# Kernel optimization log

Hardware: AMD Instinct MI355X
Metric: run time of the kernel (lower is better)

## Reference

```python
import jax, jax.numpy as jnp
import numpy as np

THRESHOLD = 0.35      # overlap_thresh
NEGPOS_RATIO = 7
VAR0, VAR1 = 0.1, 0.2  # self.variance


def make_priors():
    # Standard RetinaFace 640x640 anchor grid -> 16800 priors (cx, cy, w, h)
    img = 640
    steps = [8, 16, 32]
    min_sizes = [[16, 32], [64, 128], [256, 512]]
    out = []
    for step, ms in zip(steps, min_sizes):
        f = img // step
        ii, jj = np.meshgrid(np.arange(f), np.arange(f), indexing="ij")
        cx = ((jj + 0.5) * step / img).ravel().astype(np.float32)
        cy = ((ii + 0.5) * step / img).ravel().astype(np.float32)
        for m in ms:
            s = np.full_like(cx, m / img)
            out.append(np.stack([cx, cy, s, s], axis=-1))
    return jnp.asarray(np.concatenate(out, axis=0), dtype=jnp.float32)


def jaccard(a, b):
    # a: [O,4] point-form gt boxes, b: [P,4] point-form priors -> IoU [O,P]
    lt = jnp.maximum(a[:, None, :2], b[None, :, :2])
    rb = jnp.minimum(a[:, None, 2:], b[None, :, 2:])
    wh = jnp.clip(rb - lt, 0.0)
    inter = wh[..., 0] * wh[..., 1]
    area_a = ((a[:, 2] - a[:, 0]) * (a[:, 3] - a[:, 1]))[:, None]
    area_b = ((b[:, 2] - b[:, 0]) * (b[:, 3] - b[:, 1]))[None, :]
    return inter / (area_a + area_b - inter)


def setup_inputs() -> dict:
    key = jax.random.key(0)
    ks = jax.random.split(key, 7)
    B, P, O = 64, 16800, 64
    loc_data = jax.random.normal(ks[0], (B, P, 4), jnp.float32)
    conf_data = jax.random.normal(ks[1], (B, P, 2), jnp.float32)
    landm_data = jax.random.normal(ks[2], (B, P, 10), jnp.float32)
    priors = make_priors()
    # targets: [B, O, 15] = [xmin ymin xmax ymax | 10 landmark coords | label]
    c = jax.random.uniform(ks[3], (B, O, 2), minval=0.15, maxval=0.85)
    wh = jax.random.uniform(ks[4], (B, O, 2), minval=0.05, maxval=0.3)
    boxes = jnp.concatenate([jnp.clip(c - wh / 2, 1e-3, 0.999),
                             jnp.clip(c + wh / 2, 1e-3, 0.999)], axis=-1)
    landms = jax.random.uniform(ks[5], (B, O, 10))
    lab = jnp.where(jax.random.uniform(ks[6], (B, O, 1)) < 0.8, 1.0, -1.0)
    targets = jnp.concatenate([boxes, landms, lab], axis=-1).astype(jnp.float32)
    return {"loc_data": loc_data, "conf_data": conf_data,
            "landm_data": landm_data, "priors": priors, "targets": targets}


def _smooth_l1(x):
    ax = jnp.abs(x)
    return jnp.where(ax < 1.0, 0.5 * ax * ax, ax - 0.5)


def reference(loc_data, conf_data, landm_data, priors, targets):
    B, P, C = conf_data.shape
    O = targets.shape[1]
    priors_pf = jnp.concatenate([priors[:, :2] - priors[:, 2:] * 0.5,
                                 priors[:, :2] + priors[:, 2:] * 0.5], axis=1)

    def match_one(t):
        truths = t[:, :4]
        landms = t[:, 4:14]
        labels = t[:, 14].astype(jnp.int32)
        ov = jaccard(truths, priors_pf)               # [O,P]
        bp_ov = ov.max(axis=1)                         # best prior per truth
        bp_idx = jnp.argmax(ov, axis=1)
        valid = bp_ov >= 0.2                           # RetinaFace gt filter
        bt_ov = ov.max(axis=0)                         # best truth per prior
        bt_idx = jnp.argmax(ov, axis=0)
        # index_fill_(best_prior_idx, 2) for valid gts, ensure best prior kept
        bt_ov = bt_ov.at[bp_idx].set(jnp.where(valid, 2.0, bt_ov[bp_idx]))
        bt_idx = bt_idx.at[bp_idx].set(jnp.arange(O))
        matched = truths[bt_idx]                       # [P,4] point form
        conf = labels[bt_idx]
        conf = jnp.where(bt_ov < THRESHOLD, 0, conf)
        # encode loc target
        g_cxcy = ((matched[:, :2] + matched[:, 2:]) * 0.5 - priors[:, :2]) / (VAR0 * priors[:, 2:])
        g_wh = jnp.log((matched[:, 2:] - matched[:, :2]) / priors[:, 2:]) / VAR1
        loc = jnp.concatenate([g_cxcy, g_wh], axis=1)
        # encode landmark target (5 points)
        ml = landms[bt_idx].reshape(P, 5, 2)
        lm = ((ml - priors[:, None, :2]) / (VAR0 * priors[:, None, 2:])).reshape(P, 10)
        any_valid = jnp.any(valid)                     # early-return branch of match()
        return (jnp.where(any_valid, loc, 0.0),
                jnp.where(any_valid, conf, 0),
                jnp.where(any_valid, lm, 0.0))

    loc_t, conf_t, landm_t = jax.vmap(match_one)(targets)
    loc_t = jax.lax.stop_gradient(loc_t)       # targets built from .data in torch
    landm_t = jax.lax.stop_gradient(landm_t)

    # landmark loss over conf_t > 0
    pos1 = conf_t > 0
    N1 = jnp.maximum(pos1.sum().astype(jnp.float32), 1.0)
    loss_landm = jnp.sum(jnp.where(pos1[..., None], _smooth_l1(landm_data - landm_t), 0.0))

    # localization loss over conf_t != 0 (labels -1 and 1 both positive)
    pos = conf_t != 0
    conf_t1 = jnp.where(pos, 1, conf_t)        # conf_t[pos] = 1 -> values in {0,1}
    loss_l = jnp.sum(jnp.where(pos[..., None], _smooth_l1(loc_data - loc_t), 0.0))

    # hard negative mining
    lse = jax.nn.logsumexp(conf_data, axis=2)                       # [B,P]
    picked = jnp.take_along_axis(conf_data, conf_t1[..., None], axis=2)[..., 0]
    ce_all = lse - picked                                            # per-anchor CE
    rank_score = jnp.where(pos, 0.0, ce_all)
    loss_idx = jnp.argsort(-rank_score, axis=1)
    idx_rank = jnp.argsort(loss_idx, axis=1)
    num_pos = pos.sum(axis=1, keepdims=True)
    num_neg = jnp.minimum(NEGPOS_RATIO * num_pos, P - 1)
    neg = idx_rank < num_neg
    union = pos | neg
    loss_c = jnp.sum(jnp.where(union, ce_all, 0.0))

    N = jnp.maximum(num_pos.sum().astype(jnp.float32), 1.0)
    return loss_l / N, loss_c / N, loss_landm / N1
```

## Files before the change

kernel.cpp:

```cpp
#include <hip/hip_runtime.h>
#include <math.h>

#define B 64
#define P 16800
#define O 64
#define THRESH 0.35f
#define VALID_T 0.2f
#define HB 2048
#define HSHIFT 21
#define AREA_M 0.34f
#define CCAP 4096
#define MULT 2
#define RPB 2
#define CHB (MULT * 256)
#define NB2 ((P + CHB - 1) / CHB)
#define KD1B ((B / RPB) * NB2)
#define KCEB (B * 4)
#define KB2B (B * O / 4)
#define QG (P / 4 / 4)

__device__ __forceinline__ float smooth_l1(float x) {
    float ax = fabsf(x);
    return ax < 1.f ? 0.5f * ax * ax : ax - 0.5f;
}
__device__ __forceinline__ float lse2(float c0, float c1) {
    float m = fmaxf(c0, c1);
    return m + __logf(__expf(c0 - m) + __expf(c1 - m));
}
__device__ __forceinline__ void iou_upd(float4 t, float area_a,
                                        float px1, float py1, float px2, float py2,
                                        float area_b,
                                        float& bnum, float& bden, int& bio, int o) {
    float w = fmaxf(fminf(t.z, px2) - fmaxf(t.x, px1), 0.f);
    float h = fmaxf(fminf(t.w, py2) - fmaxf(t.y, py1), 0.f);
    float inter = w * h;
    float den = area_a + area_b - inter;
    if (inter * bden > bnum * den) { bnum = inter; bden = den; bio = o; }
}
__device__ __forceinline__ float wave_sum(float v) {
#pragma unroll
    for (int s = 32; s > 0; s >>= 1) v += __shfl_down(v, s, 64);
    return v;
}
__device__ __forceinline__ int wave_sum_i(int v) {
#pragma unroll
    for (int s = 32; s > 0; s >>= 1) v += __shfl_down(v, s, 64);
    return v;
}
__device__ __forceinline__ float wave_min(float v) {
#pragma unroll
    for (int s = 32; s > 0; s >>= 1) v = fminf(v, __shfl_xor(v, s, 64));
    return v;
}
__device__ __forceinline__ float wave_max(float v) {
#pragma unroll
    for (int s = 32; s > 0; s >>= 1) v = fmaxf(v, __shfl_xor(v, s, 64));
    return v;
}
__device__ __forceinline__ int wave_sufscan(int v, int lane) {
#pragma unroll
    for (int s = 1; s < 64; s <<= 1) {
        int o = __shfl_down(v, s, 64);
        if (lane + s < 64) v += o;
    }
    return v;
}
__device__ __forceinline__ void wave0_select(const int* h, int nb, int k,
                                             int* s_bin, int* s_kk, int tid) {
    if (tid >= 64) return;
    int lane = tid;
    int bpl = (nb + 63) >> 6;
    int b0 = lane * bpl;
    int s = 0;
    for (int i = 0; i < bpl; ++i) { int bb = b0 + i; if (bb < nb) s += h[bb]; }
    int suf = wave_sufscan(s, lane);
    int sufn = __shfl_down(suf, 1, 64);
    if (lane == 63) sufn = 0;
    if (suf >= k && sufn < k) {
        int cum = sufn;
        for (int i = bpl - 1; i >= 0; --i) {
            int bb = b0 + i; if (bb >= nb) continue;
            int hv = h[bb];
            if (cum + hv >= k) { *s_bin = bb; *s_kk = k - cum; break; }
            cum += hv;
        }
    }
}

__global__ void __launch_bounds__(256) kMain(
        const float* __restrict__ loc_data, const float* __restrict__ conf_data,
        const float* __restrict__ landm_data, const float* __restrict__ priors,
        const float* __restrict__ targets,
        unsigned char* __restrict__ pflag, float* __restrict__ rank,
        int* __restrict__ hist,
        int* __restrict__ num_pos,
        float* __restrict__ gsum, int* __restrict__ np1_tot,
        unsigned long long* __restrict__ bp_final) {
    if (blockIdx.x >= KD1B + KCEB) {
        int pair = (blockIdx.x - KD1B - KCEB) * 4 + (threadIdx.x >> 6);
        int lane = threadIdx.x & 63;
        int o = pair & (O - 1);
        int b = pair >> 6;
        const float* tt = &targets[(b * O + o) * 15];
        float tx1 = tt[0], ty1 = tt[1], tx2 = tt[2], ty2 = tt[3];
        float area_a = (tx2 - tx1) * (ty2 - ty1);
        float4 tb = make_float4(tx1, ty1, tx2, ty2);
        float bn = 0.f, bd = 1.f;
        unsigned bp = 0u;
        const int fs[6]   = {80, 80, 40, 40, 20, 20};
        const int ms[6]   = {16, 32, 64, 128, 256, 512};
        const int base[6] = {0, 6400, 12800, 14400, 16000, 16400};
#pragma unroll
        for (int c = 0; c < 6; ++c) {
            int f = fs[c];
            float inv = (float)f;
            float h = (float)ms[c] * (0.5f / 640.f);
            int j0 = (int)floorf((tx1 - h) * inv - 0.5f) - 1; if (j0 < 0) j0 = 0;
            int j1 = (int)ceilf((tx2 + h) * inv - 0.5f) + 1;  if (j1 > f - 1) j1 = f - 1;
            int i0 = (int)floorf((ty1 - h) * inv - 0.5f) - 1; if (i0 < 0) i0 = 0;
            int i1 = (int)ceilf((ty2 + h) * inv - 0.5f) + 1;  if (i1 > f - 1) i1 = f - 1;
            if (j1 < j0 || i1 < i0) continue;
            int nj = j1 - j0 + 1;
            int n = (i1 - i0 + 1) * nj;
            float rcp_nj = 1.0f / (float)nj;
            for (int idx = lane; idx < n; idx += 64) {
                int ii = (int)((float)idx * rcp_nj);
                int jj = idx - ii * nj;
                if (jj < 0) { ii--; jj += nj; } else if (jj >= nj) { ii++; jj -= nj; }
                int p = base[c] + (i0 + ii) * f + (j0 + jj);
                float4 q = ((const float4*)priors)[p];
                float px1 = q.x - q.z * 0.5f, py1 = q.y - q.w * 0.5f;
                float px2 = q.x + q.z * 0.5f, py2 = q.y + q.w * 0.5f;
                float areab = (px2 - px1) * (py2 - py1);
                float w = fmaxf(fminf(tb.z, px2) - fmaxf(tb.x, px1), 0.f);
                float hh = fmaxf(fminf(tb.w, py2) - fmaxf(tb.y, py1), 0.f);
                float inter = w * hh;
                float den = area_a + areab - inter;
                float l = bn * den, r = inter * bd;
                if (r > l) { bn = inter; bd = den; bp = (unsigned)p; }
            }
        }
#pragma unroll
        for (int s = 32; s > 0; s >>= 1) {
            float no = __shfl_xor(bn, s, 64), dd = __shfl_xor(bd, s, 64);
            unsigned po = __shfl_xor(bp, s, 64);
            float l = bn * dd, r = no * bd;
            bool take = (r > l) || (r == l && po < bp);
            if (take) { bn = no; bd = dd; bp = po; }
        }
        if (lane == 0) {
            float iou = bn / bd;
            bp_final[b * O + o] = ((unsigned long long)__float_as_uint(iou) << 32)
                                | (unsigned)(0xFFFFFFFFu - bp);
        }
        return;
    }
    if (blockIdx.x >= KD1B) {
        int cb = blockIdx.x - KD1B;
        int b = cb >> 2, q = cb & 3;
        __shared__ int lhist[HB];
        int tid = threadIdx.x;
        for (int i = tid; i < HB; i += 256) lhist[i] = 0;
        __syncthreads();
        const float4* c4 = (const float4*)(conf_data + (size_t)b * P * 2);
        uint4* r4 = (uint4*)(rank + (size_t)b * P);
        for (int i = tid; i < QG; i += 256) {
            int e = q * QG + i;
            float4 a = c4[2 * e];
            float4 c = c4[2 * e + 1];
            unsigned u0 = __float_as_uint(lse2(a.x, a.y) - a.x);
            unsigned u1 = __float_as_uint(lse2(a.z, a.w) - a.z);
            unsigned u2 = __float_as_uint(lse2(c.x, c.y) - c.x);
            unsigned u3 = __float_as_uint(lse2(c.z, c.w) - c.z);
            r4[e] = make_uint4(u0, u1, u2, u3);
            atomicAdd(&lhist[u0 >> HSHIFT], 1);
            atomicAdd(&lhist[u1 >> HSHIFT], 1);
            atomicAdd(&lhist[u2 >> HSHIFT], 1);
            atomicAdd(&lhist[u3 >> HSHIFT], 1);
        }
        __syncthreads();
        int* gh = hist + (size_t)b * HB;
        for (int i = tid; i < HB; i += 256) {
            int cgt = lhist[i];
            if (cgt) atomicAdd(&gh[i], cgt);
        }
        return;
    }
    int blk = blockIdx.x % NB2;
    int rp = blockIdx.x / NB2;
    int p0 = blk * CHB;
    __shared__ float traw[O * 15];
    __shared__ float4 t4[O];
    __shared__ float ta[O], lab[O];
    __shared__ float wredf[2][4];
    __shared__ int wredi[2][4];
    int tid = threadIdx.x;
    int wid = tid >> 6, lid = tid & 63;
    float px1[MULT], py1[MULT], px2[MULT], py2[MULT], areab[MULT];
    float4 pr4[MULT];
    bool act[MULT];
    float cbx1[MULT], cby1[MULT], cbx2[MULT], cby2[MULT], camn[MULT], camx[MULT];
#pragma unroll
    for (int mi = 0; mi < MULT; ++mi) {
        int p = p0 + mi * 256 + tid;
        act[mi] = (p < P);
        int pc = act[mi] ? p : (P - 1);
        float4 q = ((const float4*)priors)[pc];
        pr4[mi] = q;
        px1[mi] = q.x - q.z * 0.5f; py1[mi] = q.y - q.w * 0.5f;
        px2[mi] = q.x + q.z * 0.5f; py2[mi] = q.y + q.w * 0.5f;
        areab[mi] = (px2[mi] - px1[mi]) * (py2[mi] - py1[mi]);
        cbx1[mi] = wave_min(px1[mi]); cby1[mi] = wave_min(py1[mi]);
        cbx2[mi] = wave_max(px2[mi]); cby2[mi] = wave_max(py2[mi]);
        camn[mi] = wave_min(areab[mi]); camx[mi] = wave_max(areab[mi]);
    }
    for (int r = 0; r < RPB; ++r) {
        int b = rp * RPB + r;
        __syncthreads();
        if (tid < O * 15 / 4)
            ((float4*)traw)[tid] = ((const float4*)(targets + (size_t)b * O * 15))[tid];
        __syncthreads();
        if (tid < 64) {
            const float* tr = &traw[tid * 15];
            float a0 = tr[0], a1 = tr[1], a2 = tr[2], a3 = tr[3];
            t4[tid] = make_float4(a0, a1, a2, a3);
            ta[tid] = (a2 - a0) * (a3 - a1);
            lab[tid] = tr[14];
        }
        __syncthreads();
        float4 tl = t4[lid];
        float Aal = ta[lid];
        unsigned long long mk[MULT];
#pragma unroll
        for (int mi = 0; mi < MULT; ++mi) {
            bool pass = (fminf(tl.z, cbx2[mi]) - fmaxf(tl.x, cbx1[mi]) > 0.f) &&
                        (fminf(tl.w, cby2[mi]) - fmaxf(tl.y, cby1[mi]) > 0.f) &&
                        (Aal >= AREA_M * camn[mi]) && (camx[mi] >= AREA_M * Aal);
            mk[mi] = __ballot(pass);
        }
        float bnum[MULT], bden[MULT]; int bi[MULT];
#pragma unroll
        for (int mi = 0; mi < MULT; ++mi) {
            bnum[mi] = 0.f; bden[mi] = 1.f; bi[mi] = 0;
            unsigned long long mm = mk[mi];
            float Ap = areab[mi];
            while (mm) {
                int o = __ffsll(mm) - 1;
                mm &= mm - 1;
                float4 t = t4[o];
                float Aa = ta[o];
                if (Aa >= AREA_M * Ap && Ap >= AREA_M * Aa)
                    iou_upd(t, Aa, px1[mi], py1[mi], px2[mi], py2[mi], Ap,
                            bnum[mi], bden[mi], bi[mi], o);
            }
        }
        float ll = 0.f, llm = 0.f;
        int cp = 0, cp1 = 0;
#pragma unroll
        for (int mi = 0; mi < MULT; ++mi) {
            if (!act[mi]) continue;
            int p = p0 + mi * 256 + tid;
            float best = bnum[mi] / bden[mi];
            int conf = (best >= THRESH) ? (int)lab[bi[mi]] : 0;
            bool pos = conf != 0;
            pflag[(size_t)b * P + p] = pos ? 1 : 0;
            if (pos) {
                cp++;
                int ti = bi[mi];
                float cx = pr4[mi].x, cy = pr4[mi].y, sw = pr4[mi].z, sh = pr4[mi].w;
                float4 t = t4[ti];
                float gx = ((t.x + t.z) * 0.5f - cx) / (0.1f * sw);
                float gy = ((t.y + t.w) * 0.5f - cy) / (0.1f * sh);
                float gw = logf((t.z - t.x) / sw) / 0.2f;
                float gh = logf((t.w - t.y) / sh) / 0.2f;
                const float* ld = &loc_data[(size_t)(b * P + p) * 4];
                ll += smooth_l1(ld[0] - gx) + smooth_l1(ld[1] - gy) +
                      smooth_l1(ld[2] - gw) + smooth_l1(ld[3] - gh);
                if (conf > 0) {
                    cp1++;
                    const float* lmd = &landm_data[(size_t)(b * P + p) * 10];
                    const float* lmt = &traw[ti * 15 + 4];
                    for (int k5 = 0; k5 < 5; ++k5) {
                        float lx = (lmt[k5 * 2 + 0] - cx) / (0.1f * sw);
                        float ly = (lmt[k5 * 2 + 1] - cy) / (0.1f * sh);
                        llm += smooth_l1(lmd[k5 * 2 + 0] - lx) + smooth_l1(lmd[k5 * 2 + 1] - ly);
                    }
                }
            }
        }
        float s_ll = wave_sum(ll), s_llm = wave_sum(llm);
        int s_cp = wave_sum_i(cp), s_cp1 = wave_sum_i(cp1);
        if (lid == 0) {
            wredf[0][wid] = s_ll; wredf[1][wid] = s_llm;
            wredi[0][wid] = s_cp; wredi[1][wid] = s_cp1;
        }
        __syncthreads();
        if (tid == 0) {
            float ll_t = wredf[0][0] + wredf[0][1] + wredf[0][2] + wredf[0][3];
            float llm_t = wredf[1][0] + wredf[1][1] + wredf[1][2] + wredf[1][3];
            int cp_t = wredi[0][0] + wredi[0][1] + wredi[0][2] + wredi[0][3];
            int cp1_t = wredi[1][0] + wredi[1][1] + wredi[1][2] + wredi[1][3];
            if (ll_t != 0.f)  atomicAdd(&gsum[0], ll_t);
            if (llm_t != 0.f) atomicAdd(&gsum[1], llm_t);
            if (cp_t)  atomicAdd(&num_pos[b], cp_t);
            if (cp1_t) atomicAdd(np1_tot, cp1_t);
        }
    }
}

__global__ void __launch_bounds__(1024) kTail(
        const float* __restrict__ priors, const float* __restrict__ targets,
        const float* __restrict__ loc_data, const float* __restrict__ conf_data,
        const float* __restrict__ landm_data,
        const unsigned long long* __restrict__ bp_final,
        const unsigned char* __restrict__ pflag,
        const float* __restrict__ rank, const int* __restrict__ hist,
        const int* __restrict__ num_pos,
        float* __restrict__ gsum, int* __restrict__ np1_tot, int* __restrict__ np_tot,
        float* __restrict__ lossc_tot, int* __restrict__ done,
        float* __restrict__ out) {
    __shared__ __align__(16) unsigned lrow[P];
    __shared__ int lh[HB];
    __shared__ float4 t4[O];
    __shared__ float ta[O], lab[O];
    __shared__ int sp[O];
    __shared__ int hist2[256];
    __shared__ unsigned lcand[CCAP];
    __shared__ int s_np, s_bin0, s_kk0, s_bin, s_kk, s_cnt;
    __shared__ float wredf[16];
    __shared__ int wredi[16];
    __shared__ float s_cepw[16];
    __shared__ float s_sumgt;

    int b = blockIdx.x;
    int tid = threadIdx.x;
    int lane = tid & 63;
    int wv = tid >> 6;
    for (int i = tid; i < HB; i += 1024) lh[i] = hist[(size_t)b * HB + i];
    if (tid == 0) s_cnt = 0;
    int p = 0, v = 0;
    if (tid < O) {
        const float* tt = &targets[(b * O + tid) * 15];
        float4 tj = make_float4(tt[0], tt[1], tt[2], tt[3]);
        t4[tid] = tj;
        ta[tid] = (tj.z - tj.x) * (tj.w - tj.y);
        lab[tid] = tt[14];
        unsigned long long kpk = bp_final[b * O + tid];
        p = (int)(0xFFFFFFFFu - (unsigned)(kpk & 0xFFFFFFFFu));
        float iou = __uint_as_float((unsigned)(kpk >> 32));
        v = (iou >= VALID_T) ? 1 : 0;
        sp[tid] = p;
    }
    const uint4* r4 = (const uint4*)(rank + (size_t)b * P);
    for (int i = tid; i < P / 4; i += 1024) ((uint4*)lrow)[i] = r4[i];
    __syncthreads();
    const uchar4* f4v = (const uchar4*)(pflag + (size_t)b * P);
    const float2* cf2 = (const float2*)(conf_data + (size_t)b * P * 2);
    float cep = 0.f;
    for (int i = tid; i < P / 4; i += 1024) {
        uchar4 fl = f4v[i];
        if (fl.x | fl.y | fl.z | fl.w) {
#pragma unroll
            for (int kq = 0; kq < 4; ++kq) {
                unsigned char f = (kq == 0) ? fl.x : (kq == 1) ? fl.y : (kq == 2) ? fl.z : fl.w;
                if (f) {
                    int pp = i * 4 + kq;
                    unsigned old = lrow[pp];
                    lrow[pp] = 0u;
                    atomicAdd(&lh[old >> HSHIFT], -1);
                    atomicAdd(&lh[0], 1);
                    float2 cc = cf2[pp];
                    cep += lse2(cc.x, cc.y) - cc.y;
                }
            }
        }
    }
    {
        float sc = wave_sum(cep);
        if (lane == 0) s_cepw[wv] = sc;
    }
    __syncthreads();
    int dnp = 0, dn1 = 0;
    float dll = 0.f, dllm = 0.f, dce = 0.f;
    if (tid < O) {
        int j = tid;
        bool winner = true;
        for (int jj = j + 1; jj < O; ++jj)
            if (sp[jj] == p) { winner = false; break; }
        if (winner) {
            float4 q = ((const float4*)priors)[p];
            float px1 = q.x - q.z * 0.5f, py1 = q.y - q.w * 0.5f;
            float px2 = q.x + q.z * 0.5f, py2 = q.y + q.w * 0.5f;
            float areab = (px2 - px1) * (py2 - py1);
            float bnum = 0.f, bden = 1.f; int bi = 0;
            for (int o = 0; o < O; ++o) {
                float Aa = ta[o];
                if (Aa >= AREA_M * areab && areab >= AREA_M * Aa)
                    iou_upd(t4[o], Aa, px1, py1, px2, py2, areab, bnum, bden, bi, o);
            }
            float best = bnum / bden;
            float ov_new = v ? 2.0f : best;
            int conf_old = (best >= THRESH) ? (int)lab[bi] : 0;
            int conf_new = (ov_new >= THRESH) ? (int)lab[j] : 0;
            float2 c01 = ((const float2*)conf_data)[b * P + p];
            float c0 = c01.x, c1 = c01.y;
            float lse = lse2(c0, c1);
            bool po = conf_old != 0, pn = conf_new != 0;
            float ceo = lse - (po ? c1 : c0), cen = lse - (pn ? c1 : c0);
            float rvo = po ? 0.f : ceo, rvn = pn ? 0.f : cen;
            if (__float_as_uint(rvo) != __float_as_uint(rvn)) {
                lrow[p] = __float_as_uint(rvn);
                int bo = __float_as_uint(rvo) >> HSHIFT, bn = __float_as_uint(rvn) >> HSHIFT;
                if (bo != bn) { atomicAdd(&lh[bn], 1); atomicAdd(&lh[bo], -1); }
            }
            const float* ld = &loc_data[(size_t)(b * P + p) * 4];
            auto enc_ll = [&](int ti) -> float {
                float4 t = t4[ti];
                float gx = ((t.x + t.z) * 0.5f - q.x) / (0.1f * q.z);
                float gy = ((t.y + t.w) * 0.5f - q.y) / (0.1f * q.w);
                float gw = logf((t.z - t.x) / q.z) / 0.2f;
                float gh = logf((t.w - t.y) / q.w) / 0.2f;
                return smooth_l1(ld[0] - gx) + smooth_l1(ld[1] - gy) +
                       smooth_l1(ld[2] - gw) + smooth_l1(ld[3] - gh);
            };
            if (po) dll -= enc_ll(bi);
            if (pn) dll += enc_ll(j);
            dce = (pn ? cen : 0.f) - (po ? ceo : 0.f);
            dnp = (int)pn - (int)po;
            const float* lmd = &landm_data[(size_t)(b * P + p) * 10];
            auto enc_lm = [&](int ti) -> float {
                const float* lmt = &targets[(b * O + ti) * 15 + 4];
                float sum = 0.f;
                for (int k5 = 0; k5 < 5; ++k5) {
                    float lx = (lmt[k5 * 2 + 0] - q.x) / (0.1f * q.z);
                    float ly = (lmt[k5 * 2 + 1] - q.y) / (0.1f * q.w);
                    sum += smooth_l1(lmd[k5 * 2 + 0] - lx) + smooth_l1(lmd[k5 * 2 + 1] - ly);
                }
                return sum;
            };
            if (conf_old > 0) dllm -= enc_lm(bi);
            if (conf_new > 0) dllm += enc_lm(j);
            dn1 = (int)(conf_new > 0) - (int)(conf_old > 0);
        }
    }
    float pce_reg = 0.f;
    if (tid < 64) {
        float r_ll = wave_sum(dll), r_lm = wave_sum(dllm), r_ce = wave_sum(dce);
        int r_np = wave_sum_i(dnp), r_n1 = wave_sum_i(dn1);
        if (tid == 0) {
            if (r_ll != 0.f) atomicAdd(&gsum[0], r_ll);
            if (r_lm != 0.f) atomicAdd(&gsum[1], r_lm);
            float cep_tot = 0.f;
            for (int i = 0; i < 16; ++i) cep_tot += s_cepw[i];
            pce_reg = cep_tot + r_ce;
            int np = num_pos[b] + r_np;
            s_np = np;
            atomicAdd(np_tot, np);
            if (r_n1) atomicAdd(np1_tot, r_n1);
        }
    }
    __syncthreads();
    int k = s_np * 7;
    if (k > P - 1) k = P - 1;
    if (tid == 0) { s_bin0 = (k <= 0) ? -1 : 0; s_kk0 = (k <= 0) ? 0 : k; }
    if (k > 0) wave0_select(lh, HB, k, &s_bin0, &s_kk0, tid);
    __syncthreads();
    int bin = s_bin0;
    int kk0 = s_kk0;
    float topk_b = 0.f;
    if (bin >= 0) {
        if (tid < 256) hist2[tid] = 0;
        __syncthreads();
        unsigned lo_bound = ((unsigned)(bin + 1)) << HSHIFT;
        float sumgt = 0.f;
        for (int i = tid; i < P / 4; i += 1024) {
            uint4 u4 = ((const uint4*)lrow)[i];
#define TAIL_H(u) { if ((u) >= lo_bound) sumgt += __uint_as_float(u); \
                    else if (((u) >> HSHIFT) == (unsigned)bin) { \
                        int idx = atomicAdd(&s_cnt, 1); \
                        if (idx < CCAP) lcand[idx] = (u); \
                        atomicAdd(&hist2[((u) >> 13) & 255], 1); } }
            TAIL_H(u4.x) TAIL_H(u4.y) TAIL_H(u4.z) TAIL_H(u4.w)
#undef TAIL_H
        }
        float sg = wave_sum(sumgt);
        if (lane == 0) wredf[wv] = sg;
        __syncthreads();
        if (tid == 0) {
            float t = 0.f;
            for (int i = 0; i < 16; ++i) t += wredf[i];
            s_sumgt = t;
        }
        wave0_select(hist2, 256, kk0, &s_bin, &s_kk, tid);
        __syncthreads();
        unsigned pref = (((unsigned)bin) << HSHIFT) | (((unsigned)s_bin) << 13);
        unsigned resolved = (0xFFFFFFFFu << HSHIFT) | (255u << 13);
        int kk = s_kk;
        int m = s_cnt;
        bool useG = (m > CCAP);
        for (int pass = 0; pass < 2; ++pass) {
            int sh = pass == 0 ? 5 : 0;
            int nb = pass == 0 ? 256 : 32;
            if (tid < nb) hist2[tid] = 0;
            __syncthreads();
            if (!useG) {
                for (int i = tid; i < m; i += 1024) {
                    unsigned u = lcand[i];
                    if ((u & resolved) == pref) atomicAdd(&hist2[(u >> sh) & (nb - 1)], 1);
                }
            } else {
                for (int pp = tid; pp < P; pp += 1024) {
                    unsigned u = lrow[pp];
                    if ((u & resolved) == pref) atomicAdd(&hist2[(u >> sh) & (nb - 1)], 1);
                }
            }
            __syncthreads();
            wave0_select(hist2, nb, kk, &s_bin, &s_kk, tid);
            __syncthreads();
            pref |= ((unsigned)s_bin) << sh;
            resolved |= (unsigned)(nb - 1) << sh;
            kk = s_kk;
        }
        float tv = __uint_as_float(pref);
        float sumS = 0.f; int cntS = 0;
        for (int pp = tid; pp < P; pp += 1024) {
            unsigned u = lrow[pp];
            if ((u >> HSHIFT) == (unsigned)bin) {
                float val = __uint_as_float(u);
                if (val > tv) { sumS += val; cntS++; }
            }
        }
        float s2 = wave_sum(sumS); int c2 = wave_sum_i(cntS);
        if (lane == 0) { wredf[wv] = s2; wredi[wv] = c2; }
        __syncthreads();
        if (tid == 0) {
            float st = 0.f; int ct = 0;
            for (int i = 0; i < 16; ++i) { st += wredf[i]; ct += wredi[i]; }
            topk_b = s_sumgt + st + (float)(kk0 - ct) * tv;
        }
    }
    if (tid == 0) {
        atomicAdd(lossc_tot, pce_reg + topk_b);
        __threadfence();
        int old = atomicAdd(done, 1);
        if (old == B - 1) {
            float g0 = atomicAdd(&gsum[0], 0.f);
            float g1 = atomicAdd(&gsum[1], 0.f);
            float lc = atomicAdd(lossc_tot, 0.f);
            int np = atomicAdd(np_tot, 0);
            int n1 = atomicAdd(np1_tot, 0);
            float N = fmaxf((float)np, 1.f);
            float N1 = fmaxf((float)n1, 1.f);
            out[0] = g0 / N;
            out[1] = lc / N;
            out[2] = g1 / N1;
        }
    }
}

extern "C" void kernel_launch(void* const* d_in, const int* in_sizes, int n_in,
                              void* d_out, int out_size, void* d_ws, size_t ws_size,
                              hipStream_t stream) {
    const float* loc_data   = (const float*)d_in[0];
    const float* conf_data  = (const float*)d_in[1];
    const float* landm_data = (const float*)d_in[2];
    const float* priors     = (const float*)d_in[3];
    const float* targets    = (const float*)d_in[4];
    float* out = (float*)d_out;

    char* ws = (char*)d_ws;
    size_t off = 0;
    auto alloc = [&](size_t bytes) -> void* {
        void* pp = ws + off;
        off += (bytes + 255) & ~(size_t)255;
        return pp;
    };
    float* rank     = (float*)alloc((size_t)B * P * 4);
    unsigned char* pflag = (unsigned char*)alloc((size_t)B * P);
    unsigned long long* bp_final = (unsigned long long*)alloc((size_t)B * O * 8);
    size_t hist_bytes = (size_t)B * HB * 4;
    char* zbase = (char*)alloc(hist_bytes);
    int* hist = (int*)zbase;
    size_t acc_bytes = (size_t)(B * 4 + 64);
    char* acc = (char*)alloc(acc_bytes);
    int*   num_pos      = (int*)acc;
    float* gsum         = (float*)(acc + B * 4);
    int*   np1_tot      = (int*)(acc + B * 4 + 8);
    int*   np_tot       = (int*)(acc + B * 4 + 12);
    float* lossc_tot    = (float*)(acc + B * 4 + 16);
    int*   done         = (int*)(acc + B * 4 + 20);
    size_t zlen = (size_t)((acc + acc_bytes) - zbase);

    hipMemsetAsync(zbase, 0, zlen, stream);
    kMain<<<dim3(KD1B + KCEB + KB2B), dim3(256), 0, stream>>>(
        loc_data, conf_data, landm_data, priors, targets,
        pflag, rank, hist, num_pos, gsum, np1_tot, bp_final);
    kTail<<<dim3(B), dim3(1024), 0, stream>>>(priors, targets, loc_data, conf_data,
                                              landm_data, bp_final, pflag, rank, hist,
                                              num_pos, gsum, np1_tot, np_tot,
                                              lossc_tot, done, out);
}
```

Before: 168.1 us.

## Split per-batch tail kernel into fix, segmented scan, and resolve kernels

The single 64-block, 1024-thread tail kernel used to stage a whole rank row in shared memory. It is replaced by three kernels: a 256-thread fix-up kernel that patches rank/pflag in global memory and picks the coarse bin, a scan kernel that spreads the threshold-bin scan over 16 segments per batch row (1024 blocks) with ballot-aggregated candidate compaction into global memory, and a resolve kernel that finishes the radix select from the compacted candidates. This exposes far more parallelism for the full-row scan and lowers per-block shared memory, at the cost of two extra launches and extra global traffic and atomics.

```diff
diff --git a/kernel.cpp b/kernel.cpp
--- a/kernel.cpp
+++ b/kernel.cpp
@@ -18,6 +18,8 @@
 #define KCEB (B * 4)
 #define KB2B (B * O / 4)
 #define QG (P / 4 / 4)
+#define SSEG 16
+#define SLEN (P / SSEG)
 
 __device__ __forceinline__ float smooth_l1(float x) {
     float ax = fabsf(x);
@@ -308,36 +310,26 @@
     }
 }
 
-__global__ void __launch_bounds__(1024) kTail(
+__global__ void __launch_bounds__(256) kFixBin(
         const float* __restrict__ priors, const float* __restrict__ targets,
         const float* __restrict__ loc_data, const float* __restrict__ conf_data,
         const float* __restrict__ landm_data,
         const unsigned long long* __restrict__ bp_final,
-        const unsigned char* __restrict__ pflag,
-        const float* __restrict__ rank, const int* __restrict__ hist,
+        unsigned char* __restrict__ pflag, float* __restrict__ rank,
+        const int* __restrict__ hist,
         const int* __restrict__ num_pos,
         float* __restrict__ gsum, int* __restrict__ np1_tot, int* __restrict__ np_tot,
-        float* __restrict__ lossc_tot, int* __restrict__ done,
-        float* __restrict__ out) {
-    __shared__ __align__(16) unsigned lrow[P];
+        float* __restrict__ pos_ce, int* __restrict__ binArr, int* __restrict__ kkArr) {
     __shared__ int lh[HB];
     __shared__ float4 t4[O];
     __shared__ float ta[O], lab[O];
     __shared__ int sp[O];
-    __shared__ int hist2[256];
-    __shared__ unsigned lcand[CCAP];
-    __shared__ int s_np, s_bin0, s_kk0, s_bin, s_kk, s_cnt;
-    __shared__ float wredf[16];
-    __shared__ int wredi[16];
-    __shared__ float s_cepw[16];
-    __shared__ float s_sumgt;
-
+    __shared__ float s_cepw[4];
+    __shared__ int s_np, s_bin0, s_kk0;
     int b = blockIdx.x;
     int tid = threadIdx.x;
-    int lane = tid & 63;
-    int wv = tid >> 6;
-    for (int i = tid; i < HB; i += 1024) lh[i] = hist[(size_t)b * HB + i];
-    if (tid == 0) s_cnt = 0;
+    int lane = tid & 63, wv = tid >> 6;
+    for (int i = tid; i < HB; i += 256) lh[i] = hist[(size_t)b * HB + i];
     int p = 0, v = 0;
     if (tid < O) {
         const float* tt = &targets[(b * O + tid) * 15];
@@ -351,13 +343,12 @@
         v = (iou >= VALID_T) ? 1 : 0;
         sp[tid] = p;
     }
-    const uint4* r4 = (const uint4*)(rank + (size_t)b * P);
-    for (int i = tid; i < P / 4; i += 1024) ((uint4*)lrow)[i] = r4[i];
     __syncthreads();
     const uchar4* f4v = (const uchar4*)(pflag + (size_t)b * P);
+    const float* rrow = rank + (size_t)b * P;
     const float2* cf2 = (const float2*)(conf_data + (size_t)b * P * 2);
     float cep = 0.f;
-    for (int i = tid; i < P / 4; i += 1024) {
+    for (int i = tid; i < P / 4; i += 256) {
         uchar4 fl = f4v[i];
         if (fl.x | fl.y | fl.z | fl.w) {
 #pragma unroll
@@ -365,8 +356,7 @@
                 unsigned char f = (kq == 0) ? fl.x : (kq == 1) ? fl.y : (kq == 2) ? fl.z : fl.w;
                 if (f) {
                     int pp = i * 4 + kq;
-                    unsigned old = lrow[pp];
-                    lrow[pp] = 0u;
+                    unsigned old = __float_as_uint(rrow[pp]);
                     atomicAdd(&lh[old >> HSHIFT], -1);
                     atomicAdd(&lh[0], 1);
                     float2 cc = cf2[pp];
@@ -409,7 +399,8 @@
             float ceo = lse - (po ? c1 : c0), cen = lse - (pn ? c1 : c0);
             float rvo = po ? 0.f : ceo, rvn = pn ? 0.f : cen;
             if (__float_as_uint(rvo) != __float_as_uint(rvn)) {
-                lrow[p] = __float_as_uint(rvn);
+                rank[(size_t)b * P + p] = cen;
+                pflag[(size_t)b * P + p] = pn ? 1 : 0;
                 int bo = __float_as_uint(rvo) >> HSHIFT, bn = __float_as_uint(rvn) >> HSHIFT;
                 if (bo != bn) { atomicAdd(&lh[bn], 1); atomicAdd(&lh[bo], -1); }
             }
@@ -443,16 +434,14 @@
             dn1 = (int)(conf_new > 0) - (int)(conf_old > 0);
         }
     }
-    float pce_reg = 0.f;
     if (tid < 64) {
         float r_ll = wave_sum(dll), r_lm = wave_sum(dllm), r_ce = wave_sum(dce);
         int r_np = wave_sum_i(dnp), r_n1 = wave_sum_i(dn1);
         if (tid == 0) {
             if (r_ll != 0.f) atomicAdd(&gsum[0], r_ll);
             if (r_lm != 0.f) atomicAdd(&gsum[1], r_lm);
-            float cep_tot = 0.f;
-            for (int i = 0; i < 16; ++i) cep_tot += s_cepw[i];
-            pce_reg = cep_tot + r_ce;
+            float cep_tot = s_cepw[0] + s_cepw[1] + s_cepw[2] + s_cepw[3];
+            pos_ce[b] = cep_tot + r_ce;
             int np = num_pos[b] + r_np;
             s_np = np;
             atomicAdd(np_tot, np);
@@ -463,59 +452,113 @@
     int k = s_np * 7;
     if (k > P - 1) k = P - 1;
     if (tid == 0) { s_bin0 = (k <= 0) ? -1 : 0; s_kk0 = (k <= 0) ? 0 : k; }
+    __syncthreads();
     if (k > 0) wave0_select(lh, HB, k, &s_bin0, &s_kk0, tid);
     __syncthreads();
-    int bin = s_bin0;
-    int kk0 = s_kk0;
+    if (tid == 0) { binArr[b] = s_bin0; kkArr[b] = s_kk0; }
+}
+
+__global__ void __launch_bounds__(256) kScan(
+        const float* __restrict__ rank, const unsigned char* __restrict__ pflag,
+        const int* __restrict__ binArr,
+        float* __restrict__ sumgt_part, unsigned* __restrict__ cand,
+        int* __restrict__ cand_cnt, int* __restrict__ h1) {
+    int seg = blockIdx.x % SSEG;
+    int b = blockIdx.x / SSEG;
+    int bin = binArr[b];
+    if (bin < 0) return;
+    __shared__ float wred[4];
+    int t = threadIdx.x;
+    int lane = t & 63, wv = t >> 6;
+    unsigned lo_bound = ((unsigned)(bin + 1)) << HSHIFT;
+    const float* r = rank + (size_t)b * P;
+    const unsigned char* f = pflag + (size_t)b * P;
+    int* hrow = h1 + b * 256;
+    float sumgt = 0.f;
+    int pend = (seg + 1) * SLEN;
+    for (int p = seg * SLEN + t; p < pend; p += 256) {
+        unsigned u = f[p] ? 0u : __float_as_uint(r[p]);
+        bool gt = u >= lo_bound;
+        bool inb = !gt && ((u >> HSHIFT) == (unsigned)bin);
+        if (gt) sumgt += __uint_as_float(u);
+        unsigned long long mkb = __ballot(inb);
+        if (mkb) {
+            unsigned long long act = __ballot(true);
+            int ldr = __ffsll(act) - 1;
+            int cnt = __popcll(mkb);
+            int bas = 0;
+            if (lane == ldr) bas = atomicAdd(&cand_cnt[b], cnt);
+            bas = __shfl(bas, ldr, 64);
+            if (inb) {
+                int pos = bas + __popcll(mkb & ((1ull << lane) - 1ull));
+                if (pos < CCAP) cand[(size_t)b * CCAP + pos] = u;
+                atomicAdd(&hrow[(u >> 13) & 255], 1);
+            }
+        }
+    }
+    float sg = wave_sum(sumgt);
+    if (lane == 0) wred[wv] = sg;
+    __syncthreads();
+    if (t == 0) {
+        float tot = wred[0] + wred[1] + wred[2] + wred[3];
+        if (tot != 0.f) atomicAdd(&sumgt_part[b], tot);
+    }
+}
+
+__global__ void __launch_bounds__(256) kResolve(
+        const float* __restrict__ rank, const unsigned char* __restrict__ pflag,
+        const unsigned* __restrict__ cand, const int* __restrict__ cand_cnt,
+        const int* __restrict__ binArr, const int* __restrict__ kkArr,
+        const float* __restrict__ sumgt_part, const int* __restrict__ h1,
+        const float* __restrict__ pos_ce,
+        float* __restrict__ gsum, int* __restrict__ np_tot, int* __restrict__ np1_tot,
+        float* __restrict__ lossc_tot, int* __restrict__ done,
+        float* __restrict__ out) {
+    __shared__ unsigned lcand[CCAP];
+    __shared__ int hist2[256];
+    __shared__ int s_bin, s_kk;
+    __shared__ float wredf[4];
+    __shared__ int wredi[4];
+    int b = blockIdx.x;
+    int t = threadIdx.x;
+    int lane = t & 63, wv = t >> 6;
+    int bin = binArr[b];
     float topk_b = 0.f;
     if (bin >= 0) {
-        if (tid < 256) hist2[tid] = 0;
-        __syncthreads();
-        unsigned lo_bound = ((unsigned)(bin + 1)) << HSHIFT;
-        float sumgt = 0.f;
-        for (int i = tid; i < P / 4; i += 1024) {
-            uint4 u4 = ((const uint4*)lrow)[i];
-#define TAIL_H(u) { if ((u) >= lo_bound) sumgt += __uint_as_float(u); \
-                    else if (((u) >> HSHIFT) == (unsigned)bin) { \
-                        int idx = atomicAdd(&s_cnt, 1); \
-                        if (idx < CCAP) lcand[idx] = (u); \
-                        atomicAdd(&hist2[((u) >> 13) & 255], 1); } }
-            TAIL_H(u4.x) TAIL_H(u4.y) TAIL_H(u4.z) TAIL_H(u4.w)
-#undef TAIL_H
-        }
-        float sg = wave_sum(sumgt);
-        if (lane == 0) wredf[wv] = sg;
-        __syncthreads();
-        if (tid == 0) {
-            float t = 0.f;
-            for (int i = 0; i < 16; ++i) t += wredf[i];
-            s_sumgt = t;
-        }
-        wave0_select(hist2, 256, kk0, &s_bin, &s_kk, tid);
+        int m = cand_cnt[b];
+        int kk0 = kkArr[b];
+        bool useG = (m > CCAP);
+        const float* r = rank + (size_t)b * P;
+        const unsigned char* f = pflag + (size_t)b * P;
+        if (!useG) {
+            int mm = m;
+            for (int i = t; i < mm; i += 256) lcand[i] = cand[(size_t)b * CCAP + i];
+        }
+        if (t < 256) hist2[t] = h1[b * 256 + t];
+        __syncthreads();
+        wave0_select(hist2, 256, kk0, &s_bin, &s_kk, t);
         __syncthreads();
         unsigned pref = (((unsigned)bin) << HSHIFT) | (((unsigned)s_bin) << 13);
         unsigned resolved = (0xFFFFFFFFu << HSHIFT) | (255u << 13);
         int kk = s_kk;
-        int m = s_cnt;
-        bool useG = (m > CCAP);
         for (int pass = 0; pass < 2; ++pass) {
             int sh = pass == 0 ? 5 : 0;
             int nb = pass == 0 ? 256 : 32;
-            if (tid < nb) hist2[tid] = 0;
+            if (t < nb) hist2[t] = 0;
             __syncthreads();
             if (!useG) {
-                for (int i = tid; i < m; i += 1024) {
+                for (int i = t; i < m; i += 256) {
                     unsigned u = lcand[i];
                     if ((u & resolved) == pref) atomicAdd(&hist2[(u >> sh) & (nb - 1)], 1);
                 }
             } else {
-                for (int pp = tid; pp < P; pp += 1024) {
-                    unsigned u = lrow[pp];
+                for (int pp = t; pp < P; pp += 256) {
+                    unsigned u = f[pp] ? 0u : __float_as_uint(r[pp]);
                     if ((u & resolved) == pref) atomicAdd(&hist2[(u >> sh) & (nb - 1)], 1);
                 }
             }
             __syncthreads();
-            wave0_select(hist2, nb, kk, &s_bin, &s_kk, tid);
+            wave0_select(hist2, nb, kk, &s_bin, &s_kk, t);
             __syncthreads();
             pref |= ((unsigned)s_bin) << sh;
             resolved |= (unsigned)(nb - 1) << sh;
@@ -523,24 +566,31 @@
         }
         float tv = __uint_as_float(pref);
         float sumS = 0.f; int cntS = 0;
-        for (int pp = tid; pp < P; pp += 1024) {
-            unsigned u = lrow[pp];
-            if ((u >> HSHIFT) == (unsigned)bin) {
-                float val = __uint_as_float(u);
+        if (!useG) {
+            for (int i = t; i < m; i += 256) {
+                float val = __uint_as_float(lcand[i]);
                 if (val > tv) { sumS += val; cntS++; }
+            }
+        } else {
+            for (int pp = t; pp < P; pp += 256) {
+                unsigned u = f[pp] ? 0u : __float_as_uint(r[pp]);
+                if ((u >> HSHIFT) == (unsigned)bin) {
+                    float val = __uint_as_float(u);
+                    if (val > tv) { sumS += val; cntS++; }
+                }
             }
         }
         float s2 = wave_sum(sumS); int c2 = wave_sum_i(cntS);
         if (lane == 0) { wredf[wv] = s2; wredi[wv] = c2; }
         __syncthreads();
-        if (tid == 0) {
-            float st = 0.f; int ct = 0;
-            for (int i = 0; i < 16; ++i) { st += wredf[i]; ct += wredi[i]; }
-            topk_b = s_sumgt + st + (float)(kk0 - ct) * tv;
-        }
-    }
-    if (tid == 0) {
-        atomicAdd(lossc_tot, pce_reg + topk_b);
+        if (t == 0) {
+            float st = wredf[0] + wredf[1] + wredf[2] + wredf[3];
+            int ct = wredi[0] + wredi[1] + wredi[2] + wredi[3];
+            topk_b = sumgt_part[b] + st + (float)(kk0 - ct) * tv;
+        }
+    }
+    if (t == 0) {
+        atomicAdd(lossc_tot, pos_ce[b] + topk_b);
         __threadfence();
         int old = atomicAdd(done, 1);
         if (old == B - 1) {
@@ -578,25 +628,40 @@
     float* rank     = (float*)alloc((size_t)B * P * 4);
     unsigned char* pflag = (unsigned char*)alloc((size_t)B * P);
     unsigned long long* bp_final = (unsigned long long*)alloc((size_t)B * O * 8);
+    unsigned* cand  = (unsigned*)alloc((size_t)B * CCAP * 4);
+    int* binArr     = (int*)alloc(B * 4);
+    int* kkArr      = (int*)alloc(B * 4);
     size_t hist_bytes = (size_t)B * HB * 4;
     char* zbase = (char*)alloc(hist_bytes);
     int* hist = (int*)zbase;
-    size_t acc_bytes = (size_t)(B * 4 + 64);
-    char* acc = (char*)alloc(acc_bytes);
+    size_t rest_bytes = (size_t)(B * 256 * 4 + 3 * B * 4 + B * 4 + 64);
+    char* zr = (char*)alloc(rest_bytes);
+    int*   h1         = (int*)zr;
+    float* sumgt_part = (float*)(zr + B * 256 * 4);
+    int*   cand_cnt   = (int*)(zr + B * 256 * 4 + B * 4);
+    float* pos_ce     = (float*)(zr + B * 256 * 4 + 2 * B * 4);
+    char*  acc        = zr + B * 256 * 4 + 3 * B * 4;
     int*   num_pos      = (int*)acc;
-    float* gsum         = (float*)(acc + B * 4);
-    int*   np1_tot      = (int*)(acc + B * 4 + 8);
-    int*   np_tot       = (int*)(acc + B * 4 + 12);
-    float* lossc_tot    = (float*)(acc + B * 4 + 16);
-    int*   done         = (int*)(acc + B * 4 + 20);
-    size_t zlen = (size_t)((acc + acc_bytes) - zbase);
+    float* gsum         = (float*)(acc);
+    int*   np1_tot      = (int*)(acc + 8);
+    int*   np_tot       = (int*)(acc + 12);
+    float* lossc_tot    = (float*)(acc + 16);
+    int*   done         = (int*)(acc + 20);
+    (void)num_pos;
+    char* zb2 = (char*)alloc((size_t)B * 4);
+    int* num_pos2 = (int*)zb2;
+    size_t zlen = (size_t)((zb2 + B * 4) - zbase);
 
     hipMemsetAsync(zbase, 0, zlen, stream);
     kMain<<<dim3(KD1B + KCEB + KB2B), dim3(256), 0, stream>>>(
         loc_data, conf_data, landm_data, priors, targets,
-        pflag, rank, hist, num_pos, gsum, np1_tot, bp_final);
-    kTail<<<dim3(B), dim3(1024), 0, stream>>>(priors, targets, loc_data, conf_data,
-                                              landm_data, bp_final, pflag, rank, hist,
-                                              num_pos, gsum, np1_tot, np_tot,
-                                              lossc_tot, done, out);
-}
+        pflag, rank, hist, num_pos2, gsum, np1_tot, bp_final);
+    kFixBin<<<dim3(B), dim3(256), 0, stream>>>(
+        priors, targets, loc_data, conf_data, landm_data, bp_final,
+        pflag, rank, hist, num_pos2, gsum, np1_tot, np_tot, pos_ce, binArr, kkArr);
+    kScan<<<dim3(B * SSEG), dim3(256), 0, stream>>>(
+        rank, pflag, binArr, sumgt_part, cand, cand_cnt, h1);
+    kResolve<<<dim3(B), dim3(256), 0, stream>>>(
+        rank, pflag, cand, cand_cnt, binArr, kkArr, sumgt_part, h1, pos_ce,
+        gsum, np_tot, np1_tot, lossc_tot, done, out);
+}
```

New measurement: 266.6 us. 1.59x slower.
